# Performance work log

Hardware: AMD Instinct MI355X
Metric: run time of the kernel (lower is better)

Reference implementation:

```python
import jax, jax.numpy as jnp
import numpy as np

B, T, D = 4, 2048, 1024
H, KD, VD = 16, 64, 64  # num_heads, key_dim, value_dim; H*KD == D


def setup_inputs() -> dict:
    key = jax.random.key(0)
    ks = jax.random.split(key, 10)
    s = 0.02
    return {
        "q_in": jax.random.normal(ks[0], (B, T, D), jnp.float32),
        "v_in": jax.random.normal(ks[1], (B, T, D), jnp.float32),
        "Wq": jax.random.normal(ks[2], (D, H * KD), jnp.float32) * s,
        "bq": jnp.zeros((H * KD,), jnp.float32),
        "Wk": jax.random.normal(ks[3], (D, H * KD), jnp.float32) * s,
        "bk": jnp.zeros((H * KD,), jnp.float32),
        "Wv": jax.random.normal(ks[4], (D, H * VD), jnp.float32) * s,
        "bv": jnp.zeros((H * VD,), jnp.float32),
        "Wo": jax.random.normal(ks[5], (H * VD, D), jnp.float32) * s,
        "bo": jnp.zeros((D,), jnp.float32),
    }


def reference(q_in, v_in, Wq, bq, Wk, bk, Wv, bv, Wo, bo):
    # QKV projections (key defaults to value input)
    q = q_in @ Wq + bq                      # [B,T,H*KD]
    k = v_in @ Wk + bk                      # [B,T,H*KD]
    v = v_in @ Wv + bv                      # [B,T,H*VD]
    q = q.reshape(B, T, H, KD)
    k = k.reshape(B, T, H, KD)
    v = v.reshape(B, T, H, VD)
    # scaled dot-product attention, scores materialized as [B,H,Tq,Tv]
    q = q / jnp.sqrt(jnp.asarray(KD, q.dtype))
    scores = jnp.einsum('bqnh,bvnh->bnqv', q, k)
    weights = jax.nn.softmax(scores, axis=-1)
    out = jnp.einsum('bnqv,bvnh->bqnh', weights, v)  # [B,Tq,H,VD]
    out = out.reshape(B, T, H * VD)
    return out @ Wo + bo                    # [B,T,D]
```

## Files before the change

kernel.cpp:

```cpp
#include <hip/hip_runtime.h>

#define BATCH  4
#define T_SEQ  2048
#define NH     16
#define DMODEL 1024
#define HD     64

typedef float    f32x4 __attribute__((ext_vector_type(4)));
typedef _Float16 f16x8 __attribute__((ext_vector_type(8)));
typedef _Float16 f16x4 __attribute__((ext_vector_type(4)));
typedef __fp16   h16x2 __attribute__((ext_vector_type(2)));

#define LOG2E 1.44269504088896f

__device__ __forceinline__ void lds_load16(const void* g, void* l) {
  __builtin_amdgcn_global_load_lds((const __attribute__((address_space(1))) void*)g,
                                   (__attribute__((address_space(3))) void*)l, 16, 0, 0);
}

__device__ __forceinline__ f16x4 pack4_f16(float a, float b, float c, float d) {
  union { h16x2 h[2]; f16x4 f; } u;
  u.h[0] = __builtin_amdgcn_cvt_pkrtz(a, b);
  u.h[1] = __builtin_amdgcn_cvt_pkrtz(c, d);
  return u.f;
}

__device__ __forceinline__ f16x4 shflx16(f16x4 v) {
  union { f16x4 f; int i[2]; } u;
  u.f = v;
  u.i[0] = __shfl_xor(u.i[0], 16, 64);
  u.i[1] = __shfl_xor(u.i[1], 16, 64);
  return u.f;
}

#define MEMFENCE asm volatile("" ::: "memory")
#define WAITVM4  asm volatile("s_waitcnt vmcnt(4)" ::: "memory")
#define WAITVM0  asm volatile("s_waitcnt vmcnt(0)" ::: "memory")
#define PH_ENTER do { MEMFENCE; __builtin_amdgcn_s_barrier(); \
                      asm volatile("s_waitcnt lgkmcnt(0)" ::: "memory"); } while (0)
#define PH_EXIT  do { MEMFENCE; __builtin_amdgcn_s_barrier(); MEMFENCE; } while (0)

__global__ __launch_bounds__(256) void prep(
    const float* __restrict__ q_in, const float* __restrict__ v_in,
    _Float16* __restrict__ q16, _Float16* __restrict__ v16,
    const float* __restrict__ W0, const float* __restrict__ W1,
    const float* __restrict__ W2, const float* __restrict__ W3,
    _Float16* __restrict__ T0, _Float16* __restrict__ T1,
    _Float16* __restrict__ T2, _Float16* __restrict__ T3) {
  __shared__ float L[64][65];
  const int bid = blockIdx.x;
  if (bid < 16384) {
    const float* in = (bid >> 13) ? v_in : q_in;
    _Float16* out = (bid >> 13) ? v16 : q16;
    int i = (bid & 8191) * 256 + threadIdx.x;
    float4 v = ((const float4*)in)[i];
    f16x4 o = { (_Float16)v.x, (_Float16)v.y, (_Float16)v.z, (_Float16)v.w };
    ((f16x4*)out)[i] = o;
    return;
  }
  const int wb = bid - 16384;
  const float* W; _Float16* Wt;
  switch (wb >> 8) {
    case 0: W = W0; Wt = T0; break;
    case 1: W = W1; Wt = T1; break;
    case 2: W = W2; Wt = T2; break;
    default: W = W3; Wt = T3; break;
  }
  const int n0 = ((wb >> 4) & 15) * 64, k0 = (wb & 15) * 64;
  const int tx = threadIdx.x & 15, ty = threadIdx.x >> 4;
#pragma unroll
  for (int i = 0; i < 4; ++i) {
    float4 v = *(const float4*)&W[(size_t)(k0 + ty + 16 * i) * DMODEL + n0 + tx * 4];
    L[ty + 16 * i][tx * 4 + 0] = v.x;
    L[ty + 16 * i][tx * 4 + 1] = v.y;
    L[ty + 16 * i][tx * 4 + 2] = v.z;
    L[ty + 16 * i][tx * 4 + 3] = v.w;
  }
  __syncthreads();
#pragma unroll
  for (int i = 0; i < 4; ++i) {
    int n = n0 + ty + 16 * i;
    f16x4 o;
#pragma unroll
    for (int j = 0; j < 4; ++j) o[j] = (_Float16)L[tx * 4 + j][ty + 16 * i];
    *(f16x4*)&Wt[(size_t)n * DMODEL + k0 + tx * 4] = o;
  }
}

__device__ __forceinline__ void gemm256_body(
    const _Float16* __restrict__ A, const _Float16* __restrict__ Wt,
    const float* __restrict__ bias, void* __restrict__ Cout, float scale,
    int mode, _Float16* As0, _Float16* Bs0, _Float16* As1, _Float16* Bs1) {
  const int K = DMODEL;
  const int lane = threadIdx.x & 63, wave = threadIdx.x >> 6;
  const int m16 = lane & 15, quad = lane >> 4;
  const int wm = wave & 1;
  const int wn = wave >> 1;

  const int lin = blockIdx.x + blockIdx.y * gridDim.x;
  const int wg = (lin & 7) * 16 + (lin >> 3);
  const int m0 = (wg >> 2) * 256;
  const int n0 = (wg & 3) * 256;

  const int kof = (wave & 1) * 32 + quad * 8;
  const _Float16* aB[2][2]; const _Float16* bB[2][2];
#pragma unroll
  for (int h = 0; h < 2; ++h)
#pragma unroll
    for (int j = 0; j < 2; ++j) {
      int r = h * 128 + (wave >> 1) * 16 + 64 * j + m16;
      aB[h][j] = A  + (size_t)(m0 + r) * K + kof;
      bB[h][j] = Wt + (size_t)(n0 + r) * K + kof;
    }

  auto stageA = [&](_Float16* Ab, int h, int t) {
#pragma unroll
    for (int j = 0; j < 2; ++j)
      lds_load16(aB[h][j] + t * 64, Ab + (h * 16 + wave + 8 * j) * 512);
  };
  auto stageB = [&](_Float16* Bb, int h, int t) {
#pragma unroll
    for (int j = 0; j < 2; ++j)
      lds_load16(bB[h][j] + t * 64, Bb + (h * 16 + wave + 8 * j) * 512);
  };
  auto rdA = [&](const _Float16* Ab, int mi, int kh) {
    return *(const f16x8*)(Ab + (((wm * 8 + mi) * 2 + kh) * 64 + lane) * 8);
  };
  auto rdB = [&](const _Float16* Bb, int ni, int kh) {
    return *(const f16x8*)(Bb + (((wn * 4 + ni) * 2 + kh) * 64 + lane) * 8);
  };

  f32x4 acc[8][4] = {};

  auto tile_step = [&](int t, _Float16* Ac, const _Float16* Bc, _Float16* Bn) {
    f16x8 a03[4][2], a47[4][2], b01[2][2], b23[2][2];
#pragma unroll
    for (int mi = 0; mi < 4; ++mi) { a03[mi][0] = rdA(Ac, mi, 0); a03[mi][1] = rdA(Ac, mi, 1); }
#pragma unroll
    for (int ni = 0; ni < 2; ++ni) { b01[ni][0] = rdB(Bc, ni, 0); b01[ni][1] = rdB(Bc, ni, 1); }
    if (t < 15) stageB(Bn, 0, t + 1);
    PH_ENTER;
    __builtin_amdgcn_s_setprio(1);
#pragma unroll
    for (int mi = 0; mi < 4; ++mi)
#pragma unroll
      for (int ni = 0; ni < 2; ++ni)
#pragma unroll
        for (int kh = 0; kh < 2; ++kh)
          acc[mi][ni] = __builtin_amdgcn_mfma_f32_16x16x32_f16(a03[mi][kh], b01[ni][kh], acc[mi][ni], 0, 0, 0);
    __builtin_amdgcn_s_setprio(0);
    PH_EXIT;
#pragma unroll
    for (int ni = 0; ni < 2; ++ni) { b23[ni][0] = rdB(Bc, 2 + ni, 0); b23[ni][1] = rdB(Bc, 2 + ni, 1); }
    if (t < 15) stageB(Bn, 1, t + 1);
    PH_ENTER;
    __builtin_amdgcn_s_setprio(1);
#pragma unroll
    for (int mi = 0; mi < 4; ++mi)
#pragma unroll
      for (int ni = 0; ni < 2; ++ni)
#pragma unroll
        for (int kh = 0; kh < 2; ++kh)
          acc[mi][2 + ni] = __builtin_amdgcn_mfma_f32_16x16x32_f16(a03[mi][kh], b23[ni][kh], acc[mi][2 + ni], 0, 0, 0);
    __builtin_amdgcn_s_setprio(0);
    PH_EXIT;
#pragma unroll
    for (int mi = 0; mi < 4; ++mi) { a47[mi][0] = rdA(Ac, 4 + mi, 0); a47[mi][1] = rdA(Ac, 4 + mi, 1); }
    PH_ENTER;
    __builtin_amdgcn_s_setprio(1);
#pragma unroll
    for (int mi = 0; mi < 4; ++mi)
#pragma unroll
      for (int ni = 0; ni < 2; ++ni)
#pragma unroll
        for (int kh = 0; kh < 2; ++kh)
          acc[4 + mi][ni] = __builtin_amdgcn_mfma_f32_16x16x32_f16(a47[mi][kh], b01[ni][kh], acc[4 + mi][ni], 0, 0, 0);
    __builtin_amdgcn_s_setprio(0);
    PH_EXIT;
    if (t < 14) { stageA(Ac, 0, t + 2); stageA(Ac, 1, t + 2); }
    PH_ENTER;
    __builtin_amdgcn_s_setprio(1);
#pragma unroll
    for (int mi = 0; mi < 4; ++mi)
#pragma unroll
      for (int ni = 0; ni < 2; ++ni)
#pragma unroll
        for (int kh = 0; kh < 2; ++kh)
          acc[4 + mi][2 + ni] = __builtin_amdgcn_mfma_f32_16x16x32_f16(a47[mi][kh], b23[ni][kh], acc[4 + mi][2 + ni], 0, 0, 0);
    __builtin_amdgcn_s_setprio(0);
    if (t < 14)       WAITVM4;
    else if (t == 14) WAITVM0;
    MEMFENCE; __builtin_amdgcn_s_barrier(); MEMFENCE;
  };

  stageA(As0, 0, 0); stageA(As0, 1, 0);
  stageB(Bs0, 0, 0); stageB(Bs0, 1, 0);
  stageA(As1, 0, 1); stageA(As1, 1, 1);
  WAITVM4;
  MEMFENCE; __builtin_amdgcn_s_barrier(); MEMFENCE;

  for (int tp = 0; tp < 8; ++tp) {
    tile_step(2 * tp,     As0, Bs0, Bs1);
    tile_step(2 * tp + 1, As1, Bs1, Bs0);
  }

  float bv[4];
#pragma unroll
  for (int ni = 0; ni < 4; ++ni) bv[ni] = bias[n0 + wn * 64 + ni * 16 + m16];

  if (mode == 2) {
#pragma unroll
    for (int mi = 0; mi < 8; ++mi)
#pragma unroll
      for (int ni = 0; ni < 4; ++ni) {
        int row = m0 + wm * 128 + mi * 16 + quad * 4;
        int col = n0 + wn * 64 + ni * 16 + m16;
        int bb = row >> 11, tt = row & (T_SEQ - 1);
        int hh = col >> 6, dd = col & 63;
        f16x4 pv = pack4_f16(acc[mi][ni][0] + bv[ni], acc[mi][ni][1] + bv[ni],
                             acc[mi][ni][2] + bv[ni], acc[mi][ni][3] + bv[ni]);
        *(f16x4*)&((_Float16*)Cout)[(((size_t)bb * NH + hh) * HD + dd) * T_SEQ + tt] = pv;
      }
  } else if (mode == 0) {
#pragma unroll
    for (int mi = 0; mi < 8; ++mi)
#pragma unroll
      for (int r = 0; r < 4; ++r) {
        int row = m0 + wm * 128 + mi * 16 + quad * 4 + r;
#pragma unroll
        for (int ni = 0; ni < 4; ++ni) {
          int col = n0 + wn * 64 + ni * 16 + m16;
          float v = (acc[mi][ni][r] + bv[ni]) * scale;
          ((_Float16*)Cout)[(size_t)row * DMODEL + col] = (_Float16)v;
        }
      }
  } else {
#pragma unroll
    for (int mi = 0; mi < 8; ++mi)
#pragma unroll
      for (int r = 0; r < 4; ++r) {
        int row = m0 + wm * 128 + mi * 16 + quad * 4 + r;
#pragma unroll
        for (int ni = 0; ni < 4; ++ni) {
          int col = n0 + wn * 64 + ni * 16 + m16;
          ((float*)Cout)[(size_t)row * DMODEL + col] = acc[mi][ni][r] + bv[ni];
        }
      }
  }
}

__global__ __launch_bounds__(512, 2) void gemm_qkv(
    const _Float16* __restrict__ Aq, const _Float16* __restrict__ Av,
    const _Float16* __restrict__ Wq, const _Float16* __restrict__ Wk,
    const _Float16* __restrict__ Wv,
    const float* __restrict__ bq, const float* __restrict__ bk,
    const float* __restrict__ bv,
    _Float16* __restrict__ Cq, _Float16* __restrict__ Ck, _Float16* __restrict__ Cv) {
  __shared__ _Float16 As[2][16384], Bs[2][16384];
  const _Float16* A; const _Float16* Wt; const float* bias; _Float16* C;
  float scale; int mode;
  if (blockIdx.z == 0)      { A = Aq; Wt = Wq; bias = bq; C = Cq; scale = 0.125f * LOG2E; mode = 0; }
  else if (blockIdx.z == 1) { A = Av; Wt = Wk; bias = bk; C = Ck; scale = 1.f; mode = 0; }
  else                      { A = Av; Wt = Wv; bias = bv; C = Cv; scale = 1.f; mode = 2; }
  gemm256_body(A, Wt, bias, C, scale, mode, As[0], Bs[0], As[1], Bs[1]);
}

__global__ __launch_bounds__(256, 3) void gemm_out(
    const _Float16* __restrict__ A, const _Float16* __restrict__ Wt,
    const float* __restrict__ bias, float* __restrict__ Cout) {
  __shared__ _Float16 As[128 * 64], Bs[128 * 64];
  const int K = DMODEL;
  const int lane = threadIdx.x & 63, wave = threadIdx.x >> 6;
  const int bid = blockIdx.x + blockIdx.y * gridDim.x;
  const int m0 = ((bid & 7) * 8 + ((bid >> 3) & 7)) * 128;
  const int n0 = (bid >> 6) * 128;
  const int wr = (wave & 1) * 4, wc = (wave >> 1) * 4;
  const int m16 = lane & 15, quad = lane >> 4;

  const _Float16* ap[4]; const _Float16* bp[4];
#pragma unroll
  for (int j = 0; j < 4; ++j) {
    int g = wave * 4 + j;
    ap[j] = A  + (size_t)(m0 + (g >> 1) * 16 + m16) * K + (g & 1) * 32 + quad * 8;
    bp[j] = Wt + (size_t)(n0 + (g >> 1) * 16 + m16) * K + (g & 1) * 32 + quad * 8;
  }

  f32x4 acc[4][4] = {};

  for (int k0 = 0; k0 < 1024; k0 += 64) {
    __syncthreads();
#pragma unroll
    for (int j = 0; j < 4; ++j) {
      lds_load16(ap[j] + k0, As + (wave * 4 + j) * 512);
      lds_load16(bp[j] + k0, Bs + (wave * 4 + j) * 512);
    }
    __syncthreads();
#pragma unroll
    for (int s = 0; s < 2; ++s) {
      f16x8 bf[4];
#pragma unroll
      for (int ni = 0; ni < 4; ++ni)
        bf[ni] = *(const f16x8*)(Bs + (((wc + ni) * 2 + s) * 64 + lane) * 8);
#pragma unroll
      for (int mi = 0; mi < 4; ++mi) {
        f16x8 af = *(const f16x8*)(As + (((wr + mi) * 2 + s) * 64 + lane) * 8);
#pragma unroll
        for (int ni = 0; ni < 4; ++ni)
          acc[mi][ni] = __builtin_amdgcn_mfma_f32_16x16x32_f16(af, bf[ni], acc[mi][ni], 0, 0, 0);
      }
    }
  }

#pragma unroll
  for (int mi = 0; mi < 4; ++mi)
#pragma unroll
    for (int r = 0; r < 4; ++r) {
      int row = m0 + (wr + mi) * 16 + quad * 4 + r;
#pragma unroll
      for (int ni = 0; ni < 4; ++ni) {
        int col = n0 + (wc + ni) * 16 + m16;
        Cout[(size_t)row * DMODEL + col] = acc[mi][ni][r] + bias[col];
      }
    }
}

__global__ __launch_bounds__(256, 4) void attn_mfma(
    const _Float16* __restrict__ Q, const _Float16* __restrict__ Kb,
    const _Float16* __restrict__ Vt, _Float16* __restrict__ O) {
  __shared__ _Float16 Ks[2][64 * 64], Vs[2][64 * 64];

  const int lane = threadIdx.x & 63, wave = threadIdx.x >> 6;
  const int m16 = lane & 15, quad = lane >> 4;
  const int pe = quad & 1;
  const int vlane = m16 | ((((quad & 1) << 1) | (quad >> 1)) << 4);
  const int h = blockIdx.x;
  const int q0 = blockIdx.y * 128;
  const int b = blockIdx.z;
  const int wq = wave * 32;

  f16x8 qf[2][2];
#pragma unroll
  for (int mi = 0; mi < 2; ++mi)
#pragma unroll
    for (int ki = 0; ki < 2; ++ki) {
      int q = q0 + wq + mi * 16 + m16;
      qf[mi][ki] = *(const f16x8*)(Q + (((size_t)b * T_SEQ + q) * NH + h) * HD + ki * 32 + quad * 8);
    }

  const _Float16 *kp[2], *vp[2];
#pragma unroll
  for (int i = 0; i < 2; ++i) {
    int g = wave * 128 + i * 64 + lane;
    int tk = (g >> 7) * 16 + (g & 15);
    int dkof = ((g >> 6) & 1) * 32 + ((g >> 4) & 3) * 8;
    kp[i] = Kb + (((size_t)b * T_SEQ + tk) * NH + h) * HD + dkof;
    int dvof = (g >> 7) * 16 + (g & 15);
    int tv = ((g >> 6) & 1) * 32 + ((g >> 4) & 3) * 8;
    vp[i] = Vt + (((size_t)b * NH + h) * HD + dvof) * T_SEQ + tv;
  }

  auto stageKV = [&](int c, int kv) {
#pragma unroll
    for (int i = 0; i < 2; ++i) {
      lds_load16(kp[i] + (size_t)kv * (NH * HD), Ks[c] + (wave * 2 + i) * 512);
      lds_load16(vp[i] + kv, Vs[c] + (wave * 2 + i) * 512);
    }
  };

  const f16x8 onef = {(_Float16)1, (_Float16)1, (_Float16)1, (_Float16)1,
                      (_Float16)1, (_Float16)1, (_Float16)1, (_Float16)1};

  f32x4 o_acc[2][4] = {};
  f32x4 l_acc[2] = {};

  stageKV(0, 0);
  WAITVM0;
  MEMFENCE; __builtin_amdgcn_s_barrier(); MEMFENCE;

  for (int t = 0; t < 32; ++t) {
    const int c = t & 1;
    if (t < 31) stageKV(c ^ 1, (t + 1) * 64);

    f32x4 st[2][4] = {};
#pragma unroll
    for (int nt = 0; nt < 4; ++nt)
#pragma unroll
      for (int ki = 0; ki < 2; ++ki) {
        f16x8 kf = *(const f16x8*)(Ks[c] + ((nt * 2 + ki) * 64 + lane) * 8);
        __builtin_amdgcn_s_setprio(1);
#pragma unroll
        for (int mi = 0; mi < 2; ++mi)
          st[mi][nt] = __builtin_amdgcn_mfma_f32_16x16x32_f16(kf, qf[mi][ki], st[mi][nt], 0, 0, 0);
        __builtin_amdgcn_s_setprio(0);
      }

    f16x4 pex[2][4];
#pragma unroll
    for (int mi = 0; mi < 2; ++mi)
#pragma unroll
      for (int nt = 0; nt < 4; ++nt)
        pex[mi][nt] = pack4_f16(__builtin_amdgcn_exp2f(st[mi][nt][0]),
                                __builtin_amdgcn_exp2f(st[mi][nt][1]),
                                __builtin_amdgcn_exp2f(st[mi][nt][2]),
                                __builtin_amdgcn_exp2f(st[mi][nt][3]));

#pragma unroll
    for (int kt = 0; kt < 2; ++kt) {
      f16x8 pf[2];
#pragma unroll
      for (int mi = 0; mi < 2; ++mi) {
        f16x4 Aa = pex[mi][2 * kt], Bb = pex[mi][2 * kt + 1];
        f16x4 send = pe ? Aa : Bb;
        f16x4 recv = shflx16(send);
        union { f16x4 h[2]; f16x8 w; } u;
        u.h[0] = pe ? recv : Aa;
        u.h[1] = pe ? Bb : recv;
        pf[mi] = u.w;
        l_acc[mi] = __builtin_amdgcn_mfma_f32_16x16x32_f16(pf[mi], onef, l_acc[mi], 0, 0, 0);
      }
#pragma unroll
      for (int nd = 0; nd < 4; ++nd) {
        f16x8 vf = *(const f16x8*)(Vs[c] + ((nd * 2 + kt) * 64 + vlane) * 8);
        __builtin_amdgcn_s_setprio(1);
#pragma unroll
        for (int mi = 0; mi < 2; ++mi)
          o_acc[mi][nd] = __builtin_amdgcn_mfma_f32_16x16x32_f16(pf[mi], vf, o_acc[mi][nd], 0, 0, 0);
        __builtin_amdgcn_s_setprio(0);
      }
    }

    WAITVM0;
    MEMFENCE; __builtin_amdgcn_s_barrier(); MEMFENCE;
  }

#pragma unroll
  for (int mi = 0; mi < 2; ++mi)
#pragma unroll
    for (int r = 0; r < 4; ++r) {
      float inv = 1.f / l_acc[mi][r];
      int q = q0 + wq + mi * 16 + quad * 4 + r;
#pragma unroll
      for (int nd = 0; nd < 4; ++nd) {
        int d = nd * 16 + m16;
        O[(((size_t)b * T_SEQ + q) * NH + h) * HD + d] = (_Float16)(o_acc[mi][nd][r] * inv);
      }
    }
}

extern "C" void kernel_launch(void* const* d_in, const int* in_sizes, int n_in,
                              void* d_out, int out_size, void* d_ws, size_t ws_size,
                              hipStream_t stream) {
  const float* q_in = (const float*)d_in[0];
  const float* v_in = (const float*)d_in[1];
  const float* Wq   = (const float*)d_in[2];
  const float* bq   = (const float*)d_in[3];
  const float* Wk   = (const float*)d_in[4];
  const float* bk   = (const float*)d_in[5];
  const float* Wv   = (const float*)d_in[6];
  const float* bv   = (const float*)d_in[7];
  const float* Wo   = (const float*)d_in[8];
  const float* bo   = (const float*)d_in[9];
  float* out = (float*)d_out;

  const size_t MB = 1u << 20;
  char* ws = (char*)d_ws;
  _Float16* q16  = (_Float16*)(ws);
  _Float16* v16  = (_Float16*)(ws + 16 * MB);
  _Float16* qbuf = (_Float16*)(ws + 32 * MB);
  _Float16* kbuf = (_Float16*)(ws + 48 * MB);
  _Float16* vtb  = (_Float16*)(ws + 64 * MB);
  _Float16* Wqt  = (_Float16*)(ws + 80 * MB);
  _Float16* Wkt  = (_Float16*)(ws + 82 * MB);
  _Float16* Wvt  = (_Float16*)(ws + 84 * MB);
  _Float16* Wot  = (_Float16*)(ws + 86 * MB);

  prep<<<dim3(16384 + 1024), 256, 0, stream>>>(q_in, v_in, q16, v16,
                                               Wq, Wk, Wv, Wo, Wqt, Wkt, Wvt, Wot);

  gemm_qkv<<<dim3(4, 32, 3), 512, 0, stream>>>(q16, v16, Wqt, Wkt, Wvt, bq, bk, bv,
                                               qbuf, kbuf, vtb);

  attn_mfma<<<dim3(16, 16, 4), 256, 0, stream>>>(qbuf, kbuf, vtb, qbuf);

  gemm_out<<<dim3(8, 64), 256, 0, stream>>>(qbuf, Wot, bo, out);
}
```

Baseline: 341.2 us.

## Shrink QKV GEMM tile to 256x128 with 4x2 wave layout

Changes the QKV projection GEMM from 256x256 output tiles to 256x128 tiles. Waves are rearranged 4x2, each wave holds a 4x4 accumulator set, the B-tile LDS buffers are halved, and the grid is doubled with a new XCD-aware tile mapping. The aim is more workgroups and less register and LDS pressure, which may raise occupancy and balance load across CUs. The cost is lower arithmetic intensity per tile, since each A tile is now loaded twice.

```diff
diff --git a/kernel.cpp b/kernel.cpp
--- a/kernel.cpp
+++ b/kernel.cpp
@@ -87,58 +87,56 @@
   }
 }
 
-__device__ __forceinline__ void gemm256_body(
+__device__ __forceinline__ void gemmqkv_body(
     const _Float16* __restrict__ A, const _Float16* __restrict__ Wt,
     const float* __restrict__ bias, void* __restrict__ Cout, float scale,
     int mode, _Float16* As0, _Float16* Bs0, _Float16* As1, _Float16* Bs1) {
   const int K = DMODEL;
   const int lane = threadIdx.x & 63, wave = threadIdx.x >> 6;
   const int m16 = lane & 15, quad = lane >> 4;
-  const int wm = wave & 1;
-  const int wn = wave >> 1;
+  const int wm = wave & 3;
+  const int wn = wave >> 2;
 
   const int lin = blockIdx.x + blockIdx.y * gridDim.x;
-  const int wg = (lin & 7) * 16 + (lin >> 3);
-  const int m0 = (wg >> 2) * 256;
-  const int n0 = (wg & 3) * 256;
-
-  const int kof = (wave & 1) * 32 + quad * 8;
-  const _Float16* aB[2][2]; const _Float16* bB[2][2];
-#pragma unroll
-  for (int h = 0; h < 2; ++h)
-#pragma unroll
-    for (int j = 0; j < 2; ++j) {
-      int r = h * 128 + (wave >> 1) * 16 + 64 * j + m16;
-      aB[h][j] = A  + (size_t)(m0 + r) * K + kof;
-      bB[h][j] = Wt + (size_t)(n0 + r) * K + kof;
-    }
-
-  auto stageA = [&](_Float16* Ab, int h, int t) {
+  const int xcd = lin & 7, idx = lin >> 3;
+  const int m0 = (xcd * 4 + (idx & 3)) * 256;
+  const int n0 = (idx >> 2) * 128;
+
+  const _Float16* apg[4];
+#pragma unroll
+  for (int j = 0; j < 4; ++j)
+    apg[j] = A + (size_t)(m0 + (wave * 2 + (j >> 1)) * 16 + m16) * K + (j & 1) * 32 + quad * 8;
+  const _Float16* bpg[2];
+#pragma unroll
+  for (int j = 0; j < 2; ++j)
+    bpg[j] = Wt + (size_t)(n0 + wave * 16 + m16) * K + j * 32 + quad * 8;
+
+  auto stageA = [&](_Float16* Ab, int t) {
+#pragma unroll
+    for (int j = 0; j < 4; ++j)
+      lds_load16(apg[j] + t * 64, Ab + (wave * 4 + j) * 512);
+  };
+  auto stageB = [&](_Float16* Bb, int t) {
 #pragma unroll
     for (int j = 0; j < 2; ++j)
-      lds_load16(aB[h][j] + t * 64, Ab + (h * 16 + wave + 8 * j) * 512);
-  };
-  auto stageB = [&](_Float16* Bb, int h, int t) {
-#pragma unroll
-    for (int j = 0; j < 2; ++j)
-      lds_load16(bB[h][j] + t * 64, Bb + (h * 16 + wave + 8 * j) * 512);
+      lds_load16(bpg[j] + t * 64, Bb + (wave * 2 + j) * 512);
   };
   auto rdA = [&](const _Float16* Ab, int mi, int kh) {
-    return *(const f16x8*)(Ab + (((wm * 8 + mi) * 2 + kh) * 64 + lane) * 8);
+    return *(const f16x8*)(Ab + (((wm * 4 + mi) * 2 + kh) * 64 + lane) * 8);
   };
   auto rdB = [&](const _Float16* Bb, int ni, int kh) {
     return *(const f16x8*)(Bb + (((wn * 4 + ni) * 2 + kh) * 64 + lane) * 8);
   };
 
-  f32x4 acc[8][4] = {};
+  f32x4 acc[4][4] = {};
 
   auto tile_step = [&](int t, _Float16* Ac, const _Float16* Bc, _Float16* Bn) {
-    f16x8 a03[4][2], a47[4][2], b01[2][2], b23[2][2];
-#pragma unroll
-    for (int mi = 0; mi < 4; ++mi) { a03[mi][0] = rdA(Ac, mi, 0); a03[mi][1] = rdA(Ac, mi, 1); }
+    f16x8 af[4][2], b01[2][2], b23[2][2];
+#pragma unroll
+    for (int mi = 0; mi < 4; ++mi) { af[mi][0] = rdA(Ac, mi, 0); af[mi][1] = rdA(Ac, mi, 1); }
 #pragma unroll
     for (int ni = 0; ni < 2; ++ni) { b01[ni][0] = rdB(Bc, ni, 0); b01[ni][1] = rdB(Bc, ni, 1); }
-    if (t < 15) stageB(Bn, 0, t + 1);
+    if (t < 15) stageB(Bn, t + 1);
     PH_ENTER;
     __builtin_amdgcn_s_setprio(1);
 #pragma unroll
@@ -147,12 +145,12 @@
       for (int ni = 0; ni < 2; ++ni)
 #pragma unroll
         for (int kh = 0; kh < 2; ++kh)
-          acc[mi][ni] = __builtin_amdgcn_mfma_f32_16x16x32_f16(a03[mi][kh], b01[ni][kh], acc[mi][ni], 0, 0, 0);
+          acc[mi][ni] = __builtin_amdgcn_mfma_f32_16x16x32_f16(af[mi][kh], b01[ni][kh], acc[mi][ni], 0, 0, 0);
     __builtin_amdgcn_s_setprio(0);
     PH_EXIT;
 #pragma unroll
     for (int ni = 0; ni < 2; ++ni) { b23[ni][0] = rdB(Bc, 2 + ni, 0); b23[ni][1] = rdB(Bc, 2 + ni, 1); }
-    if (t < 15) stageB(Bn, 1, t + 1);
+    if (t < 14) stageA(Ac, t + 2);
     PH_ENTER;
     __builtin_amdgcn_s_setprio(1);
 #pragma unroll
@@ -161,41 +159,14 @@
       for (int ni = 0; ni < 2; ++ni)
 #pragma unroll
         for (int kh = 0; kh < 2; ++kh)
-          acc[mi][2 + ni] = __builtin_amdgcn_mfma_f32_16x16x32_f16(a03[mi][kh], b23[ni][kh], acc[mi][2 + ni], 0, 0, 0);
-    __builtin_amdgcn_s_setprio(0);
-    PH_EXIT;
-#pragma unroll
-    for (int mi = 0; mi < 4; ++mi) { a47[mi][0] = rdA(Ac, 4 + mi, 0); a47[mi][1] = rdA(Ac, 4 + mi, 1); }
-    PH_ENTER;
-    __builtin_amdgcn_s_setprio(1);
-#pragma unroll
-    for (int mi = 0; mi < 4; ++mi)
-#pragma unroll
-      for (int ni = 0; ni < 2; ++ni)
-#pragma unroll
-        for (int kh = 0; kh < 2; ++kh)
-          acc[4 + mi][ni] = __builtin_amdgcn_mfma_f32_16x16x32_f16(a47[mi][kh], b01[ni][kh], acc[4 + mi][ni], 0, 0, 0);
-    __builtin_amdgcn_s_setprio(0);
-    PH_EXIT;
-    if (t < 14) { stageA(Ac, 0, t + 2); stageA(Ac, 1, t + 2); }
-    PH_ENTER;
-    __builtin_amdgcn_s_setprio(1);
-#pragma unroll
-    for (int mi = 0; mi < 4; ++mi)
-#pragma unroll
-      for (int ni = 0; ni < 2; ++ni)
-#pragma unroll
-        for (int kh = 0; kh < 2; ++kh)
-          acc[4 + mi][2 + ni] = __builtin_amdgcn_mfma_f32_16x16x32_f16(a47[mi][kh], b23[ni][kh], acc[4 + mi][2 + ni], 0, 0, 0);
+          acc[mi][2 + ni] = __builtin_amdgcn_mfma_f32_16x16x32_f16(af[mi][kh], b23[ni][kh], acc[mi][2 + ni], 0, 0, 0);
     __builtin_amdgcn_s_setprio(0);
     if (t < 14)       WAITVM4;
     else if (t == 14) WAITVM0;
     MEMFENCE; __builtin_amdgcn_s_barrier(); MEMFENCE;
   };
 
-  stageA(As0, 0, 0); stageA(As0, 1, 0);
-  stageB(Bs0, 0, 0); stageB(Bs0, 1, 0);
-  stageA(As1, 0, 1); stageA(As1, 1, 1);
+  stageA(As0, 0); stageB(Bs0, 0); stageA(As1, 1);
   WAITVM4;
   MEMFENCE; __builtin_amdgcn_s_barrier(); MEMFENCE;
 
@@ -210,10 +181,10 @@
 
   if (mode == 2) {
 #pragma unroll
-    for (int mi = 0; mi < 8; ++mi)
+    for (int mi = 0; mi < 4; ++mi)
 #pragma unroll
       for (int ni = 0; ni < 4; ++ni) {
-        int row = m0 + wm * 128 + mi * 16 + quad * 4;
+        int row = m0 + (wm * 4 + mi) * 16 + quad * 4;
         int col = n0 + wn * 64 + ni * 16 + m16;
         int bb = row >> 11, tt = row & (T_SEQ - 1);
         int hh = col >> 6, dd = col & 63;
@@ -221,29 +192,17 @@
                              acc[mi][ni][2] + bv[ni], acc[mi][ni][3] + bv[ni]);
         *(f16x4*)&((_Float16*)Cout)[(((size_t)bb * NH + hh) * HD + dd) * T_SEQ + tt] = pv;
       }
-  } else if (mode == 0) {
-#pragma unroll
-    for (int mi = 0; mi < 8; ++mi)
+  } else {
+#pragma unroll
+    for (int mi = 0; mi < 4; ++mi)
 #pragma unroll
       for (int r = 0; r < 4; ++r) {
-        int row = m0 + wm * 128 + mi * 16 + quad * 4 + r;
+        int row = m0 + (wm * 4 + mi) * 16 + quad * 4 + r;
 #pragma unroll
         for (int ni = 0; ni < 4; ++ni) {
           int col = n0 + wn * 64 + ni * 16 + m16;
           float v = (acc[mi][ni][r] + bv[ni]) * scale;
           ((_Float16*)Cout)[(size_t)row * DMODEL + col] = (_Float16)v;
-        }
-      }
-  } else {
-#pragma unroll
-    for (int mi = 0; mi < 8; ++mi)
-#pragma unroll
-      for (int r = 0; r < 4; ++r) {
-        int row = m0 + wm * 128 + mi * 16 + quad * 4 + r;
-#pragma unroll
-        for (int ni = 0; ni < 4; ++ni) {
-          int col = n0 + wn * 64 + ni * 16 + m16;
-          ((float*)Cout)[(size_t)row * DMODEL + col] = acc[mi][ni][r] + bv[ni];
         }
       }
   }
@@ -256,13 +215,14 @@
     const float* __restrict__ bq, const float* __restrict__ bk,
     const float* __restrict__ bv,
     _Float16* __restrict__ Cq, _Float16* __restrict__ Ck, _Float16* __restrict__ Cv) {
-  __shared__ _Float16 As[2][16384], Bs[2][16384];
+  __shared__ _Float16 As[2][16384];
+  __shared__ _Float16 Bs[2][8192];
   const _Float16* A; const _Float16* Wt; const float* bias; _Float16* C;
   float scale; int mode;
   if (blockIdx.z == 0)      { A = Aq; Wt = Wq; bias = bq; C = Cq; scale = 0.125f * LOG2E; mode = 0; }
   else if (blockIdx.z == 1) { A = Av; Wt = Wk; bias = bk; C = Ck; scale = 1.f; mode = 0; }
   else                      { A = Av; Wt = Wv; bias = bv; C = Cv; scale = 1.f; mode = 2; }
-  gemm256_body(A, Wt, bias, C, scale, mode, As[0], Bs[0], As[1], Bs[1]);
+  gemmqkv_body(A, Wt, bias, C, scale, mode, As[0], Bs[0], As[1], Bs[1]);
 }
 
 __global__ __launch_bounds__(256, 3) void gemm_out(
@@ -477,7 +437,7 @@
   prep<<<dim3(16384 + 1024), 256, 0, stream>>>(q_in, v_in, q16, v16,
                                                Wq, Wk, Wv, Wo, Wqt, Wkt, Wvt, Wot);
 
-  gemm_qkv<<<dim3(4, 32, 3), 512, 0, stream>>>(q16, v16, Wqt, Wkt, Wvt, bq, bk, bv,
+  gemm_qkv<<<dim3(8, 32, 3), 512, 0, stream>>>(q16, v16, Wqt, Wkt, Wvt, bq, bk, bv,
                                                qbuf, kbuf, vtb);
 
   attn_mfma<<<dim3(16, 16, 4), 256, 0, stream>>>(qbuf, kbuf, vtb, qbuf);
```

After: 370.1 us. 8.5% more time.
